# Kernel optimization log

Hardware: AMD Instinct MI355X
Metric: run time of the kernel (lower is better)

The kernel has to match this reference:

```python
import jax, jax.numpy as jnp
import numpy as np

D_MODEL = 1024
D_STATE = 16
EXPAND = 2
D_HEAD = 64
D_CONV = 4
FFN = 2816
NORMALIZE_BC = True
D_INNER = EXPAND * D_MODEL          # 2048
N_HEADS = D_INNER // D_HEAD         # 32
EPS = 1e-6


def _rmsnorm(x, w):
    v = jnp.mean(x * x, axis=-1, keepdims=True)
    return x * jax.lax.rsqrt(v + EPS) * w


def _mixer(x, in_proj_w, conv_w, conv_b, A_log, dt_bias, D, out_proj_w):
    b, l, _ = x.shape
    zxbcdt = x @ in_proj_w.T  # (b, l, 2*D_INNER + 2*D_STATE + N_HEADS)
    z, xBC, dt_raw = jnp.split(zxbcdt, [D_INNER, 2 * D_INNER + 2 * D_STATE], axis=-1)
    # causal depthwise conv over (u, B, C) channels
    xp = jnp.pad(xBC, ((0, 0), (D_CONV - 1, 0), (0, 0)))
    y = conv_b + sum(xp[:, k:k + l, :] * conv_w[:, k] for k in range(D_CONV))
    xBC = jax.nn.silu(y)
    u, Bm, Cm = jnp.split(xBC, [D_INNER, D_INNER + D_STATE], axis=-1)
    if NORMALIZE_BC:
        Bm = Bm / (jnp.linalg.norm(Bm, axis=-1, keepdims=True) + EPS)
        Cm = Cm / (jnp.linalg.norm(Cm, axis=-1, keepdims=True) + EPS)
    dt = jax.nn.softplus(dt_raw + dt_bias)          # (b, l, h)
    A = jnp.exp(A_log)                              # (h, n) oscillator frequencies >= 0
    u = u.reshape(b, l, N_HEADS, D_HEAD)

    # LinOSS implicit (IM) discretization of z' = -A y + B u ; y' = z
    #   S  = 1/(1 + dt^2 A)
    #   w_k = S*(w_{k-1} - dt*A*y_{k-1} + dt*B u_k)
    #   y_k = y_{k-1} + dt*w_k ;  out_k = C y_k + D u_k
    def step(carry, inp):
        w, ys = carry                               # each (b, h, dh, n)
        dt_t, B_t, C_t, u_t = inp                   # (b,h),(b,n),(b,n),(b,h,dh)
        S = 1.0 / (1.0 + (dt_t[:, :, None] ** 2) * A[None])   # (b,h,n)
        Sb = S[:, :, None, :]
        dtb = dt_t[:, :, None, None]
        Ab = A[None, :, None, :]
        Bu = B_t[:, None, None, :] * u_t[..., None]            # (b,h,dh,n)
        w = Sb * (w - dtb * Ab * ys + dtb * Bu)
        ys = ys + dtb * w
        o = jnp.einsum('bhdn,bn->bhd', ys, C_t)
        return (w, ys), o

    init = (jnp.zeros((b, N_HEADS, D_HEAD, D_STATE), x.dtype),
            jnp.zeros((b, N_HEADS, D_HEAD, D_STATE), x.dtype))
    xs = (dt.transpose(1, 0, 2), Bm.transpose(1, 0, 2),
          Cm.transpose(1, 0, 2), u.transpose(1, 0, 2, 3))
    _, ys = jax.lax.scan(step, init, xs)            # (l, b, h, dh)
    ys = ys.transpose(1, 0, 2, 3) + D[None, None, :, None] * u
    out = ys.reshape(b, l, D_INNER) * jax.nn.silu(z)
    return out @ out_proj_w.T


def setup_inputs() -> dict:
    key = jax.random.key(0)
    ks = jax.random.split(key, 12)
    B, L = 4, 2048
    proj_dim = 2 * D_INNER + 2 * D_STATE + N_HEADS
    conv_ch = D_INNER + 2 * D_STATE
    s = lambda k, shape, sc: jax.random.normal(k, shape, jnp.float32) * sc
    return {
        "x": s(ks[0], (B, L, D_MODEL), 1.0),
        "norm1_w": jnp.ones((D_MODEL,), jnp.float32),
        "in_proj_w": s(ks[1], (proj_dim, D_MODEL), D_MODEL ** -0.5),
        "conv_w": s(ks[2], (conv_ch, D_CONV), 0.3),
        "conv_b": jnp.zeros((conv_ch,), jnp.float32),
        "A_log": s(ks[3], (N_HEADS, D_STATE), 0.5),
        "dt_bias": s(ks[4], (N_HEADS,), 0.5),
        "D": s(ks[5], (N_HEADS,), 1.0),
        "out_proj_w": s(ks[6], (D_MODEL, D_INNER), D_INNER ** -0.5),
        "norm2_w": jnp.ones((D_MODEL,), jnp.float32),
        "gate_w": s(ks[7], (FFN, D_MODEL), D_MODEL ** -0.5),
        "up_w": s(ks[8], (FFN, D_MODEL), D_MODEL ** -0.5),
        "down_w": s(ks[9], (D_MODEL, FFN), FFN ** -0.5),
    }


def reference(x, norm1_w, in_proj_w, conv_w, conv_b, A_log, dt_bias, D,
              out_proj_w, norm2_w, gate_w, up_w, down_w):
    h = x + _mixer(_rmsnorm(x, norm1_w), in_proj_w, conv_w, conv_b,
                   A_log, dt_bias, D, out_proj_w)
    hn = _rmsnorm(h, norm2_w)
    ffn = (jax.nn.silu(hn @ gate_w.T) * (hn @ up_w.T)) @ down_w.T
    return h + ffn
```

## Files before the change

### kernel.cpp

```cpp
#include <hip/hip_runtime.h>
#include <hip/hip_bf16.h>

#define D_MODEL   1024
#define D_STATE   16
#define D_HEAD    64
#define D_CONV    4
#define FFN_DIM   2816
#define D_INNER   2048
#define N_HEADS   32
#define BATCH     4
#define SEQ       2048
#define ROWS      (BATCH*SEQ)
#define PROJ_DIM  4160
#define PROJ_PAD  4352
#define CONV_CH   2080
#define CH        128
#define NCH       (SEQ/CH)

typedef __bf16 bf16x8 __attribute__((ext_vector_type(8)));
typedef float  f32x4  __attribute__((ext_vector_type(4)));

__device__ __forceinline__ float siluf(float x) { return x / (1.0f + __expf(-x)); }

#define SBAR() do { asm volatile("" ::: "memory"); __builtin_amdgcn_s_barrier(); asm volatile("" ::: "memory"); } while (0)
#define LGKM0() asm volatile("s_waitcnt lgkmcnt(0)" ::: "memory")
#define VMCNT4() asm volatile("s_waitcnt vmcnt(4)" ::: "memory")
#define VMCNT2() asm volatile("s_waitcnt vmcnt(2)" ::: "memory")
#define VMCNT0() asm volatile("s_waitcnt vmcnt(0)" ::: "memory")

__global__ void cvt_k(const float* __restrict__ src, __hip_bfloat16* __restrict__ dst, int n) {
  int i = blockIdx.x * blockDim.x + threadIdx.x;
  if (i < n) dst[i] = __float2bfloat16(src[i]);
}

__global__ void cvt_pad_k(const float* __restrict__ src, __hip_bfloat16* __restrict__ dst) {
  int i = blockIdx.x * blockDim.x + threadIdx.x;
  if (i >= PROJ_PAD * D_MODEL) return;
  int row = i >> 10;
  dst[i] = (row < PROJ_DIM) ? __float2bfloat16(src[i]) : __float2bfloat16(0.0f);
}

__global__ __launch_bounds__(256) void rmsnorm_k(const float* __restrict__ x,
                                                 const float* __restrict__ w,
                                                 __hip_bfloat16* __restrict__ out,
                                                 float* __restrict__ outf) {
  int row = blockIdx.x;
  int t = threadIdx.x;
  const float* xr = x + (size_t)row * D_MODEL;
  float4 v = ((const float4*)xr)[t];
  float ss = v.x*v.x + v.y*v.y + v.z*v.z + v.w*v.w;
  #pragma unroll
  for (int o = 32; o > 0; o >>= 1) ss += __shfl_xor(ss, o);
  __shared__ float red[4];
  if ((t & 63) == 0) red[t >> 6] = ss;
  __syncthreads();
  ss = red[0] + red[1] + red[2] + red[3];
  float scale = rsqrtf(ss * (1.0f / D_MODEL) + 1e-6f);
  float4 wv = ((const float4*)w)[t];
  float4 r;
  r.x = v.x * scale * wv.x; r.y = v.y * scale * wv.y;
  r.z = v.z * scale * wv.z; r.w = v.w * scale * wv.w;
  __hip_bfloat16* orow = out + (size_t)row * D_MODEL + t * 4;
  orow[0] = __float2bfloat16(r.x);
  orow[1] = __float2bfloat16(r.y);
  orow[2] = __float2bfloat16(r.z);
  orow[3] = __float2bfloat16(r.w);
  if (outf) ((float4*)(outf + (size_t)row * D_MODEL))[t] = r;
}

__global__ __launch_bounds__(256) void dtproj_k(const float* __restrict__ xn,
                                                const float* __restrict__ wi,
                                                const float* __restrict__ dtb,
                                                float* __restrict__ dtT) {
  const int r0 = blockIdx.x * 4;
  const int t  = threadIdx.x;
  const int hh  = t >> 3;
  const int seg = t & 7;

  __shared__ float xs[4][D_MODEL];
  #pragma unroll
  for (int i = 0; i < 4; ++i)
    ((float4*)&xs[i][0])[t] = ((const float4*)(xn + (size_t)(r0 + i) * D_MODEL))[t];
  __syncthreads();

  const float4* w4 = (const float4*)(wi + (size_t)(2 * D_INNER + 2 * D_STATE + hh) * D_MODEL) + seg * 32;
  const float4* x0 = (const float4*)&xs[0][0] + seg * 32;
  const float4* x1 = (const float4*)&xs[1][0] + seg * 32;
  const float4* x2 = (const float4*)&xs[2][0] + seg * 32;
  const float4* x3 = (const float4*)&xs[3][0] + seg * 32;
  float a0 = 0.f, a1 = 0.f, a2 = 0.f, a3 = 0.f;
  #pragma unroll 8
  for (int k = 0; k < 32; ++k) {
    float4 wv = w4[k];
    float4 v0 = x0[k], v1 = x1[k], v2 = x2[k], v3 = x3[k];
    a0 = fmaf(wv.x, v0.x, fmaf(wv.y, v0.y, fmaf(wv.z, v0.z, fmaf(wv.w, v0.w, a0))));
    a1 = fmaf(wv.x, v1.x, fmaf(wv.y, v1.y, fmaf(wv.z, v1.z, fmaf(wv.w, v1.w, a1))));
    a2 = fmaf(wv.x, v2.x, fmaf(wv.y, v2.y, fmaf(wv.z, v2.z, fmaf(wv.w, v2.w, a2))));
    a3 = fmaf(wv.x, v3.x, fmaf(wv.y, v3.y, fmaf(wv.z, v3.z, fmaf(wv.w, v3.w, a3))));
  }
  #pragma unroll
  for (int m = 1; m < 8; m <<= 1) {
    a0 += __shfl_xor(a0, m);
    a1 += __shfl_xor(a1, m);
    a2 += __shfl_xor(a2, m);
    a3 += __shfl_xor(a3, m);
  }
  if (seg == 0) {
    float bias = dtb[hh];
    float v[4] = {a0, a1, a2, a3};
    #pragma unroll
    for (int i = 0; i < 4; ++i) {
      float xv = v[i] + bias;
      dtT[(size_t)hh * ROWS + r0 + i] = (xv > 20.f) ? xv : log1pf(__expf(xv));
    }
  }
}

template<int EPI>
__global__ __launch_bounds__(512, 2) void gemm8(
    const __hip_bfloat16* __restrict__ A,
    const __hip_bfloat16* __restrict__ Bw,
    float* __restrict__ Cf,
    __hip_bfloat16* __restrict__ Cb,
    const float* __restrict__ add_src,
    int M, int N, int K)
{
  extern __shared__ char lds[];
  const int nwg = (M >> 8) * (N >> 8);
  int bid = blockIdx.x;
  bid = (bid & 7) * (nwg >> 3) + (bid >> 3);
  const int ntn = N >> 8;
  const int bm = (bid / ntn) << 8;
  const int bn = (bid % ntn) << 8;

  const int tid  = threadIdx.x;
  const int wid  = tid >> 6;
  const int lane = tid & 63;
  const int wm = wid >> 2;
  const int wn = wid & 3;
  const int r16 = lane & 15;
  const int kg  = lane >> 4;

  const int rb = ((r16 << 6) + (kg << 4)) ^ ((r16 & 8) << 2);

  const int s_sub = tid >> 6;
  const int s_w   = (tid & 63) << 4;
  const int s_wp  = s_w ^ ((((s_w) >> 9) & 1) << 5);
  const int s_row = ((s_sub >> 1) << 4) + (s_wp >> 6);
  const int s_col = ((s_sub & 1) << 5) + ((s_wp >> 1) & 31);

  auto stage = [&](int buf, int mat, int half, int c, int kt) {
    const __hip_bfloat16* src = (mat == 0)
        ? A  + (size_t)(bm + half * 128 + c * 64 + s_row) * K + kt * 64 + s_col
        : Bw + (size_t)(bn + half * 128 + c * 64 + s_row) * K + kt * 64 + s_col;
    char* dst = lds + buf * 65536 + mat * 32768 + half * 16384 + c * 8192 + tid * 16;
    __builtin_amdgcn_global_load_lds((const __attribute__((address_space(1))) unsigned int*)src,
                                     (__attribute__((address_space(3))) unsigned int*)dst,
                                     16, 0, 0);
  };

  f32x4 acc[8][4] = {};
  bf16x8 af[4][2], bfr[4][2];

  const int NT = K >> 6;
  stage(0,0,0,0,0); stage(0,0,0,1,0); stage(0,0,1,0,0); stage(0,0,1,1,0);
  stage(0,1,0,0,0); stage(0,1,0,1,0); stage(0,1,1,0,0); stage(0,1,1,1,0);
  __syncthreads();

  for (int kt = 0; kt < NT; ++kt) {
    const int buf = kt & 1, nbuf = buf ^ 1;
    const bool st = (kt + 1 < NT);
    const char* Ab = lds + buf * 65536 + wm * 16384;
    const char* Bb = lds + buf * 65536 + 32768 + (wn >> 1) * 16384 + (wn & 1) * 8192;

    #pragma unroll
    for (int mi2 = 0; mi2 < 4; ++mi2)
      #pragma unroll
      for (int kk = 0; kk < 2; ++kk)
        af[mi2][kk] = *(const bf16x8*)(Ab + (mi2 * 2 + kk) * 1024 + rb);
    #pragma unroll
    for (int ni = 0; ni < 2; ++ni)
      #pragma unroll
      for (int kk = 0; kk < 2; ++kk)
        bfr[ni][kk] = *(const bf16x8*)(Bb + (ni * 2 + kk) * 1024 + rb);
    if (st) { stage(nbuf,1,0,0,kt+1); stage(nbuf,1,0,1,kt+1); }
    SBAR(); LGKM0();
    __builtin_amdgcn_s_setprio(1);
    #pragma unroll
    for (int mi2 = 0; mi2 < 4; ++mi2)
      #pragma unroll
      for (int ni = 0; ni < 2; ++ni)
        #pragma unroll
        for (int kk = 0; kk < 2; ++kk)
          acc[mi2][ni] = __builtin_amdgcn_mfma_f32_16x16x32_bf16(af[mi2][kk], bfr[ni][kk], acc[mi2][ni], 0, 0, 0);
    __builtin_amdgcn_s_setprio(0);
    SBAR();

    #pragma unroll
    for (int ni = 2; ni < 4; ++ni)
      #pragma unroll
      for (int kk = 0; kk < 2; ++kk)
        bfr[ni][kk] = *(const bf16x8*)(Bb + (ni * 2 + kk) * 1024 + rb);
    if (st) { stage(nbuf,1,1,0,kt+1); stage(nbuf,1,1,1,kt+1); }
    SBAR(); LGKM0();
    __builtin_amdgcn_s_setprio(1);
    #pragma unroll
    for (int mi2 = 0; mi2 < 4; ++mi2)
      #pragma unroll
      for (int ni = 2; ni < 4; ++ni)
        #pragma unroll
        for (int kk = 0; kk < 2; ++kk)
          acc[mi2][ni] = __builtin_amdgcn_mfma_f32_16x16x32_bf16(af[mi2][kk], bfr[ni][kk], acc[mi2][ni], 0, 0, 0);
    __builtin_amdgcn_s_setprio(0);
    if (st) { VMCNT4(); } else { VMCNT0(); }
    SBAR();

    #pragma unroll
    for (int mi2 = 0; mi2 < 4; ++mi2)
      #pragma unroll
      for (int kk = 0; kk < 2; ++kk)
        af[mi2][kk] = *(const bf16x8*)(Ab + ((4 + mi2) * 2 + kk) * 1024 + rb);
    if (st) { stage(nbuf,0,0,0,kt+1); stage(nbuf,0,1,0,kt+1); }
    SBAR(); LGKM0();
    __builtin_amdgcn_s_setprio(1);
    #pragma unroll
    for (int mi2 = 0; mi2 < 4; ++mi2)
      #pragma unroll
      for (int ni = 0; ni < 2; ++ni)
        #pragma unroll
        for (int kk = 0; kk < 2; ++kk)
          acc[4 + mi2][ni] = __builtin_amdgcn_mfma_f32_16x16x32_bf16(af[mi2][kk], bfr[ni][kk], acc[4 + mi2][ni], 0, 0, 0);
    __builtin_amdgcn_s_setprio(0);
    SBAR();

    if (st) { stage(nbuf,0,0,1,kt+1); stage(nbuf,0,1,1,kt+1); }
    SBAR(); LGKM0();
    __builtin_amdgcn_s_setprio(1);
    #pragma unroll
    for (int mi2 = 0; mi2 < 4; ++mi2)
      #pragma unroll
      for (int ni = 2; ni < 4; ++ni)
        #pragma unroll
        for (int kk = 0; kk < 2; ++kk)
          acc[4 + mi2][ni] = __builtin_amdgcn_mfma_f32_16x16x32_bf16(af[mi2][kk], bfr[ni][kk], acc[4 + mi2][ni], 0, 0, 0);
    __builtin_amdgcn_s_setprio(0);
    VMCNT2();
    SBAR();
  }

  #pragma unroll
  for (int mi = 0; mi < 8; ++mi) {
    #pragma unroll
    for (int ni = 0; ni < 4; ++ni) {
      #pragma unroll
      for (int j = 0; j < 4; ++j) {
        int r = bm + wm * 128 + mi * 16 + kg * 4 + j;
        int c = bn + wn * 64 + ni * 16 + r16;
        size_t idx = (size_t)r * N + c;
        float v = acc[mi][ni][j];
        if constexpr (EPI == 0) {
          Cf[idx] = v;
        } else if constexpr (EPI == 1) {
          Cf[idx] = v + add_src[idx];
        } else if constexpr (EPI == 2) {
          Cb[idx] = __float2bfloat16(siluf(v));
        } else if constexpr (EPI == 3) {
          Cb[idx] = __float2bfloat16(v * __bfloat162float(Cb[idx]));
        }
      }
    }
  }
}

template<int EPI>
__global__ __launch_bounds__(512, 2) void gemm8B(
    const __hip_bfloat16* __restrict__ A,
    const __hip_bfloat16* __restrict__ Bw,
    float* __restrict__ Cf,
    __hip_bfloat16* __restrict__ Cb,
    const float* __restrict__ add_src,
    int M, int N, int K)
{
  extern __shared__ char lds[];
  const int nwg = (M >> 8) * (N >> 7);
  int bid = blockIdx.x;
  bid = (bid & 7) * (nwg >> 3) + (bid >> 3);
  const int ntn = N >> 7;
  const int bm = (bid / ntn) << 8;
  const int bn = (bid % ntn) << 7;

  const int tid  = threadIdx.x;
  const int wid  = tid >> 6;
  const int lane = tid & 63;
  const int wm = wid >> 2;
  const int wn = wid & 3;
  const int r16 = lane & 15;
  const int kg  = lane >> 4;

  const int rb = ((r16 << 6) + (kg << 4)) ^ ((r16 & 8) << 2);

  const int s_sub = tid >> 6;
  const int s_w   = (tid & 63) << 4;
  const int s_wp  = s_w ^ ((((s_w) >> 9) & 1) << 5);
  const int s_row = ((s_sub >> 1) << 4) + (s_wp >> 6);
  const int s_col = ((s_sub & 1) << 5) + ((s_wp >> 1) & 31);

  auto stageA = [&](int buf, int half, int c, int kt) {
    const __hip_bfloat16* src = A + (size_t)(bm + half * 128 + c * 64 + s_row) * K + kt * 64 + s_col;
    char* dst = lds + buf * 65536 + half * 16384 + c * 8192 + tid * 16;
    __builtin_amdgcn_global_load_lds((const __attribute__((address_space(1))) unsigned int*)src,
                                     (__attribute__((address_space(3))) unsigned int*)dst,
                                     16, 0, 0);
  };
  auto stageB = [&](int buf, int c, int kt) {
    const __hip_bfloat16* src = Bw + (size_t)(bn + c * 64 + s_row) * K + kt * 64 + s_col;
    char* dst = lds + buf * 65536 + 32768 + c * 8192 + tid * 16;
    __builtin_amdgcn_global_load_lds((const __attribute__((address_space(1))) unsigned int*)src,
                                     (__attribute__((address_space(3))) unsigned int*)dst,
                                     16, 0, 0);
  };

  f32x4 acc[8][2] = {};
  bf16x8 af[4][2], bfr[2][2];

  const int NT = K >> 6;
  stageB(0,0,0); stageB(0,1,0);
  stageA(0,0,0,0); stageA(0,1,0,0); stageA(0,0,1,0); stageA(0,1,1,0);
  __syncthreads();

  for (int kt = 0; kt < NT; ++kt) {
    const int buf = kt & 1, nbuf = buf ^ 1;
    const bool st = (kt + 1 < NT);
    const char* Ab = lds + buf * 65536 + wm * 16384;
    const char* Bb = lds + buf * 65536 + 32768 + (wn >> 1) * 8192 + (wn & 1) * 4096;

    #pragma unroll
    for (int mi2 = 0; mi2 < 4; ++mi2)
      #pragma unroll
      for (int kk = 0; kk < 2; ++kk)
        af[mi2][kk] = *(const bf16x8*)(Ab + (mi2 * 2 + kk) * 1024 + rb);
    #pragma unroll
    for (int ni = 0; ni < 2; ++ni)
      #pragma unroll
      for (int kk = 0; kk < 2; ++kk)
        bfr[ni][kk] = *(const bf16x8*)(Bb + (ni * 2 + kk) * 1024 + rb);
    if (st) { stageB(nbuf,0,kt+1); stageB(nbuf,1,kt+1); stageA(nbuf,0,0,kt+1); stageA(nbuf,1,0,kt+1); }
    SBAR(); LGKM0();
    __builtin_amdgcn_s_setprio(1);
    #pragma unroll
    for (int mi2 = 0; mi2 < 4; ++mi2)
      #pragma unroll
      for (int ni = 0; ni < 2; ++ni)
        #pragma unroll
        for (int kk = 0; kk < 2; ++kk)
          acc[mi2][ni] = __builtin_amdgcn_mfma_f32_16x16x32_bf16(af[mi2][kk], bfr[ni][kk], acc[mi2][ni], 0, 0, 0);
    __builtin_amdgcn_s_setprio(0);
    if (st) { VMCNT4(); } else { VMCNT0(); }
    SBAR();

    #pragma unroll
    for (int mi2 = 0; mi2 < 4; ++mi2)
      #pragma unroll
      for (int kk = 0; kk < 2; ++kk)
        af[mi2][kk] = *(const bf16x8*)(Ab + ((4 + mi2) * 2 + kk) * 1024 + rb);
    if (st) { stageA(nbuf,0,1,kt+1); stageA(nbuf,1,1,kt+1); }
    SBAR(); LGKM0();
    __builtin_amdgcn_s_setprio(1);
    #pragma unroll
    for (int mi2 = 0; mi2 < 4; ++mi2)
      #pragma unroll
      for (int ni = 0; ni < 2; ++ni)
        #pragma unroll
        for (int kk = 0; kk < 2; ++kk)
          acc[4 + mi2][ni] = __builtin_amdgcn_mfma_f32_16x16x32_bf16(af[mi2][kk], bfr[ni][kk], acc[4 + mi2][ni], 0, 0, 0);
    __builtin_amdgcn_s_setprio(0);
    VMCNT2();
    SBAR();
  }

  #pragma unroll
  for (int mi = 0; mi < 8; ++mi) {
    #pragma unroll
    for (int ni = 0; ni < 2; ++ni) {
      #pragma unroll
      for (int j = 0; j < 4; ++j) {
        int r = bm + wm * 128 + mi * 16 + kg * 4 + j;
        int c = bn + wn * 32 + ni * 16 + r16;
        size_t idx = (size_t)r * N + c;
        float v = acc[mi][ni][j];
        if constexpr (EPI == 0) {
          Cf[idx] = v;
        } else if constexpr (EPI == 1) {
          Cf[idx] = v + add_src[idx];
        } else if constexpr (EPI == 2) {
          Cb[idx] = __float2bfloat16(siluf(v));
        } else if constexpr (EPI == 3) {
          Cb[idx] = __float2bfloat16(v * __bfloat162float(Cb[idx]));
        }
      }
    }
  }
}

__global__ __launch_bounds__(256) void bcdt_k(const float* __restrict__ zx,
                                              const float* __restrict__ cw,
                                              const float* __restrict__ cb,
                                              float* __restrict__ bc) {
  int t = threadIdx.x;
  int r = blockIdx.x * 8 + (t >> 5);
  int ch = t & 31;
  int l = r & (SEQ - 1);
  int c = D_INNER + ch;
  float acc = cb[c];
  #pragma unroll
  for (int k = 0; k < 4; ++k) {
    int lp = l - 3 + k;
    if (lp >= 0)
      acc = fmaf(zx[(size_t)(r - 3 + k) * PROJ_PAD + 2 * D_INNER + ch], cw[c * 4 + k], acc);
  }
  acc = siluf(acc);
  float ss = acc * acc;
  ss += __shfl_xor(ss, 1);
  ss += __shfl_xor(ss, 2);
  ss += __shfl_xor(ss, 4);
  ss += __shfl_xor(ss, 8);
  bc[r * 32 + ch] = acc / (sqrtf(ss) + 1e-6f);
}

__global__ __launch_bounds__(256) void pk_k(const float* __restrict__ dtT,
                                            const float* __restrict__ A_log,
                                            float* __restrict__ Pm) {
  int bh = blockIdx.x;
  int h = bh & 31;
  int t = threadIdx.x;
  int ch = t >> 4, n = t & 15;
  float a = __expf(A_log[h * 16 + n]);
  const float* dtp = dtT + (size_t)h * ROWS + (size_t)(bh >> 5) * SEQ + ch * CH;
  float p00 = 1.f, p01 = 0.f, p10 = 0.f, p11 = 1.f;
  for (int l = 0; l < CH; ++l) {
    float dt = dtp[l];
    float s  = 1.0f / fmaf(dt * dt, a, 1.0f);
    float m00 = s;
    float m01 = -dt * a * s;
    float m10 = dt * s;
    float m11 = fmaf(-dt * a, m10, 1.0f);
    float q00 = fmaf(m00, p00, m01 * p10);
    float q01 = fmaf(m00, p01, m01 * p11);
    float q10 = fmaf(m10, p00, m11 * p10);
    float q11 = fmaf(m10, p01, m11 * p11);
    p00 = q00; p01 = q01; p10 = q10; p11 = q11;
  }
  float4 v = {p00, p01, p10, p11};
  *(float4*)&Pm[(((size_t)bh * NCH + ch) * 16 + n) * 4] = v;
}

__global__ __launch_bounds__(256) void prop_k(const float* __restrict__ Pm,
                                              const float* __restrict__ pend,
                                              float* __restrict__ sinit) {
  int gid = blockIdx.x * 256 + threadIdx.x;
  int n  = gid & 15;
  int d  = (gid >> 4) & 63;
  int bh = gid >> 10;
  float s0 = 0.f, s1 = 0.f;
  for (int c = 0; c < NCH; ++c) {
    size_t i2 = (((size_t)bh * NCH + c) * 64 + d) * 16 + n;
    *(float2*)&sinit[i2 * 2] = make_float2(s0, s1);
    float4 P  = *(const float4*)&Pm[(((size_t)bh * NCH + c) * 16 + n) * 4];
    float2 pe = *(const float2*)&pend[i2 * 2];
    float t0 = fmaf(P.x, s0, fmaf(P.y, s1, pe.x));
    float t1 = fmaf(P.z, s0, fmaf(P.w, s1, pe.y));
    s0 = t0; s1 = t1;
  }
}

#define T_TILE 16
#define TPC (CH / T_TILE)
template<int PHASE>
__global__ __launch_bounds__(128) void scan_k(
    const float* __restrict__ zx, const float* __restrict__ bcb,
    const float* __restrict__ dtT, const float* __restrict__ A_log,
    const float* __restrict__ Dp, const float* __restrict__ cw,
    const float* __restrict__ cb, float* __restrict__ states,
    __hip_bfloat16* __restrict__ po)
{
  const int blk  = blockIdx.x;
  const int half = blk & 1;
  const int ch   = (blk >> 1) & 15;
  const int h    = (blk >> 5) & 31;
  const int b    = blk >> 10;
  const int bh   = b * 32 + h;
  const int tid  = threadIdx.x;
  const int wv   = tid >> 6;
  const int lane = tid & 63;
  const int d16  = lane & 15;
  const int ng   = lane >> 4;
  const int n0   = ng * 4;
  const int dl   = half * 32 + wv * 16 + d16;
  const int dcol = h * 64 + dl;
  const size_t rowbase = (size_t)b * SEQ + (size_t)ch * CH;

  __shared__ float xz [2][T_TILE][64];
  __shared__ float bct[2][T_TILE][32];
  __shared__ float st [2][T_TILE][32];
  __shared__ float dtt[2][T_TILE];
  __shared__ float aexp[16];
  __shared__ float opart[T_TILE][32][4];

  if (tid < 16) aexp[tid] = __expf(A_log[h * 16 + tid]);

  const float Dh = Dp[h];
  const float c0 = cw[dcol * 4 + 0], c1 = cw[dcol * 4 + 1];
  const float c2 = cw[dcol * 4 + 2], c3 = cw[dcol * 4 + 3];
  const float cbv = cb[dcol];

  auto stage = [&](int tile, int buf) {
    const size_t r0 = rowbase + (size_t)tile * T_TILE;
    #pragma unroll
    for (int i = 0; i < 2; ++i) {
      int lr = 8 * i + 4 * wv + (lane >> 4);
      int c4 = (lane & 15) * 4;
      int col = (c4 < 32) ? (h * 64 + half * 32 + c4)
                          : (D_INNER + h * 64 + half * 32 + (c4 - 32));
      const float* g = zx + (r0 + lr) * PROJ_PAD + col;
      float* l = &xz[buf][0][0] + (8 * i + 4 * wv) * 64 + (lane & 15) * 4;
      __builtin_amdgcn_global_load_lds((const __attribute__((address_space(1))) unsigned int*)g,
                                       (__attribute__((address_space(3))) unsigned int*)l,
                                       16, 0, 0);
    }
    {
      int lr = 8 * wv + (lane >> 3);
      const float* g = bcb + (r0 + lr) * 32 + (lane & 7) * 4;
      float* l = &bct[buf][0][0] + 8 * wv * 32 + (lane & 7) * 4;
      __builtin_amdgcn_global_load_lds((const __attribute__((address_space(1))) unsigned int*)g,
                                       (__attribute__((address_space(3))) unsigned int*)l,
                                       16, 0, 0);
    }
  };

  auto sprep = [&](int buf, float dtn) {
    #pragma unroll
    for (int i = 0; i < 2; ++i) {
      int idx = tid + 128 * i;
      int row = idx >> 4, n = idx & 15;
      float dv = __shfl(dtn, row);
      float a  = aexp[n];
      st[buf][row][n]      = 1.0f / fmaf(dv * dv, a, 1.0f);
      st[buf][row][16 + n] = dv * a;
    }
  };

  stage(0, 0);
  float dtn = 0.f;
  if (lane < 16) dtn = dtT[(size_t)h * ROWS + rowbase + lane];
  __syncthreads();
  if (tid < 16) dtt[0][tid] = dtn;
  sprep(0, dtn);
  __syncthreads();

  float w[4], ys[4];
  if constexpr (PHASE == 1) {
    #pragma unroll
    for (int j = 0; j < 4; ++j) { w[j] = 0.f; ys[j] = 0.f; }
  } else {
    #pragma unroll
    for (int j = 0; j < 4; ++j) {
      size_t i2 = (((size_t)bh * NCH + ch) * 64 + dl) * 16 + (n0 + j);
      float2 s = *(const float2*)&states[i2 * 2];
      w[j] = s.x; ys[j] = s.y;
    }
  }
  float xw1 = 0.f, xw2 = 0.f, xw3 = 0.f;
  if (ch > 0) {
    const float* xb = zx + rowbase * PROJ_PAD + D_INNER + dcol;
    xw1 = xb[-3 * PROJ_PAD];
    xw2 = xb[-2 * PROJ_PAD];
    xw3 = xb[-1 * PROJ_PAD];
  }
  int cur = 0;

  for (int t = 0; t < TPC; ++t) {
    if (t + 1 < TPC) {
      stage(t + 1, cur ^ 1);
      if (lane < 16) dtn = dtT[(size_t)h * ROWS + rowbase + (size_t)(t + 1) * T_TILE + lane];
    }
    #pragma unroll 4
    for (int l = 0; l < T_TILE; ++l) {
      float xl  = xz[cur][l][32 + wv * 16 + d16];
      float dtv = dtt[cur][l];
      f32x4 Sv = *(const f32x4*)&st [cur][l][n0];
      f32x4 Av = *(const f32x4*)&st [cur][l][16 + n0];
      f32x4 Bv = *(const f32x4*)&bct[cur][l][n0];
      float cacc = fmaf(c3, xl, fmaf(c2, xw3, fmaf(c1, xw2, fmaf(c0, xw1, cbv))));
      float uv = siluf(cacc);
      xw1 = xw2; xw2 = xw3; xw3 = xl;
      float du = dtv * uv;
      if constexpr (PHASE == 3) {
        f32x4 Cv = *(const f32x4*)&bct[cur][l][16 + n0];
        float o = 0.f;
        #pragma unroll
        for (int j = 0; j < 4; ++j) {
          float tmp = fmaf(-Av[j], ys[j], w[j]);
          tmp = fmaf(du, Bv[j], tmp);
          w[j] = Sv[j] * tmp;
          ys[j] = fmaf(dtv, w[j], ys[j]);
          o = fmaf(ys[j], Cv[j], o);
        }
        float ofin = (ng == 0) ? fmaf(Dh, uv, o) : o;
        opart[l][wv * 16 + d16][ng] = ofin;
      } else {
        #pragma unroll
        for (int j = 0; j < 4; ++j) {
          float tmp = fmaf(-Av[j], ys[j], w[j]);
          tmp = fmaf(du, Bv[j], tmp);
          w[j] = Sv[j] * tmp;
          ys[j] = fmaf(dtv, w[j], ys[j]);
        }
      }
    }
    if constexpr (PHASE == 3) {
      #pragma unroll
      for (int i = 0; i < 4; ++i) {
        int l  = (lane >> 4) + 4 * i;
        int dd = wv * 16 + d16;
        f32x4 op = *(const f32x4*)&opart[l][dd][0];
        float zv = xz[cur][l][dd];
        float yv = (op[0] + op[1]) + (op[2] + op[3]);
        po[(rowbase + (size_t)t * T_TILE + l) * D_INNER + (h * 64 + half * 32 + dd)] =
            __float2bfloat16(yv * siluf(zv));
      }
    }
    __syncthreads();
    if (t + 1 < TPC) {
      if (tid < 16) dtt[cur ^ 1][tid] = dtn;
      sprep(cur ^ 1, dtn);
      __syncthreads();
    }
    cur ^= 1;
  }

  if constexpr (PHASE == 1) {
    #pragma unroll
    for (int j = 0; j < 4; ++j) {
      size_t i2 = (((size_t)bh * NCH + ch) * 64 + dl) * 16 + (n0 + j);
      *(float2*)&states[i2 * 2] = make_float2(w[j], ys[j]);
    }
  }
}

extern "C" void kernel_launch(void* const* d_in, const int* in_sizes, int n_in,
                              void* d_out, int out_size, void* d_ws, size_t ws_size,
                              hipStream_t stream) {
  const float* x     = (const float*)d_in[0];
  const float* n1w   = (const float*)d_in[1];
  const float* wi    = (const float*)d_in[2];
  const float* cw    = (const float*)d_in[3];
  const float* cb    = (const float*)d_in[4];
  const float* A_log = (const float*)d_in[5];
  const float* dtb   = (const float*)d_in[6];
  const float* Dp    = (const float*)d_in[7];
  const float* wo    = (const float*)d_in[8];
  const float* n2w   = (const float*)d_in[9];
  const float* wg    = (const float*)d_in[10];
  const float* wu    = (const float*)d_in[11];
  const float* wd    = (const float*)d_in[12];
  float* out = (float*)d_out;

  char* p = (char*)d_ws;
  auto take = [&](size_t b) { char* q = p; p += (b + 255) & ~(size_t)255; return q; };
  __hip_bfloat16* wbi  = (__hip_bfloat16*)take((size_t)PROJ_PAD * D_MODEL * 2);
  __hip_bfloat16* wbo  = (__hip_bfloat16*)take((size_t)D_MODEL * D_INNER * 2);
  __hip_bfloat16* wbg  = (__hip_bfloat16*)take((size_t)FFN_DIM * D_MODEL * 2);
  __hip_bfloat16* wbu  = (__hip_bfloat16*)take((size_t)FFN_DIM * D_MODEL * 2);
  __hip_bfloat16* wbd  = (__hip_bfloat16*)take((size_t)D_MODEL * FFN_DIM * 2);
  __hip_bfloat16* h0b  = (__hip_bfloat16*)take((size_t)ROWS * D_MODEL * 2);
  float*          zx   = (float*)take((size_t)ROWS * PROJ_PAD * 4);
  float*          bcb  = (float*)take((size_t)ROWS * 32 * 4);
  float*          dtT  = (float*)take((size_t)ROWS * 32 * 4);
  __hip_bfloat16* po   = (__hip_bfloat16*)take((size_t)ROWS * D_INNER * 2);
  float*          pend = (float*)take((size_t)128 * NCH * 64 * 16 * 2 * 4);
  float*          sini = (float*)take((size_t)128 * NCH * 64 * 16 * 2 * 4);
  float*          Pm   = (float*)take((size_t)128 * NCH * 16 * 4 * 4);
  float*          h0f  = (float*)zx;
  float*          h    = (float*)zx;
  __hip_bfloat16* gact = (__hip_bfloat16*)((char*)zx + 33554432);

  hipFuncSetAttribute(reinterpret_cast<const void*>(&gemm8<0>),  hipFuncAttributeMaxDynamicSharedMemorySize, 131072);
  hipFuncSetAttribute(reinterpret_cast<const void*>(&gemm8<2>),  hipFuncAttributeMaxDynamicSharedMemorySize, 131072);
  hipFuncSetAttribute(reinterpret_cast<const void*>(&gemm8<3>),  hipFuncAttributeMaxDynamicSharedMemorySize, 131072);
  hipFuncSetAttribute(reinterpret_cast<const void*>(&gemm8B<1>), hipFuncAttributeMaxDynamicSharedMemorySize, 131072);

  cvt_pad_k<<<(PROJ_PAD * D_MODEL + 255) / 256, 256, 0, stream>>>(wi, wbi);
  cvt_k<<<(D_MODEL * D_INNER + 255) / 256, 256, 0, stream>>>(wo, wbo, D_MODEL * D_INNER);
  cvt_k<<<(FFN_DIM * D_MODEL + 255) / 256, 256, 0, stream>>>(wg, wbg, FFN_DIM * D_MODEL);
  cvt_k<<<(FFN_DIM * D_MODEL + 255) / 256, 256, 0, stream>>>(wu, wbu, FFN_DIM * D_MODEL);
  cvt_k<<<(FFN_DIM * D_MODEL + 255) / 256, 256, 0, stream>>>(wd, wbd, FFN_DIM * D_MODEL);

  rmsnorm_k<<<ROWS, 256, 0, stream>>>(x, n1w, h0b, h0f);
  dtproj_k<<<ROWS / 4, 256, 0, stream>>>(h0f, wi, dtb, dtT);
  gemm8<0><<<(ROWS / 256) * (PROJ_PAD / 256), 512, 131072, stream>>>(h0b, wbi, zx, nullptr, nullptr,
                                                                     ROWS, PROJ_PAD, D_MODEL);
  bcdt_k<<<ROWS / 8, 256, 0, stream>>>(zx, cw, cb, bcb);
  pk_k<<<BATCH * N_HEADS, 256, 0, stream>>>(dtT, A_log, Pm);
  scan_k<1><<<BATCH * N_HEADS * NCH * 2, 128, 0, stream>>>(zx, bcb, dtT, A_log, Dp, cw, cb, pend, nullptr);
  prop_k<<<BATCH * N_HEADS * 64 * 16 / 256, 256, 0, stream>>>(Pm, pend, sini);
  scan_k<3><<<BATCH * N_HEADS * NCH * 2, 128, 0, stream>>>(zx, bcb, dtT, A_log, Dp, cw, cb, sini, po);
  gemm8B<1><<<(ROWS / 256) * (D_MODEL / 128), 512, 131072, stream>>>(po, wbo, h, nullptr, x,
                                                                     ROWS, D_MODEL, D_INNER);
  rmsnorm_k<<<ROWS, 256, 0, stream>>>(h, n2w, h0b, nullptr);
  gemm8<2><<<(ROWS / 256) * (FFN_DIM / 256), 512, 131072, stream>>>(h0b, wbg, nullptr, gact, nullptr,
                                                                    ROWS, FFN_DIM, D_MODEL);
  gemm8<3><<<(ROWS / 256) * (FFN_DIM / 256), 512, 131072, stream>>>(h0b, wbu, nullptr, gact, nullptr,
                                                                    ROWS, FFN_DIM, D_MODEL);
  gemm8B<1><<<(ROWS / 256) * (D_MODEL / 128), 512, 131072, stream>>>(gact, wbd, out, nullptr, h,
                                                                     ROWS, D_MODEL, FFN_DIM);
}
```

Baseline: 711.5 us.

## Precompute conv+SiLU of u into bf16 buffer and simplify scan staging

Adds a standalone kernel that computes the causal depthwise conv and SiLU for the u channels once and stores the result as bf16 in the output buffer. Both scan phases then stage that bf16 u instead of recomputing the conv from fp32 projection columns, and phase 1 no longer loads z at all. The scan also keeps exp(A) in registers instead of in shared memory and uses packed two-wide float math for the recurrence. In exchange it adds an extra pass over the projection output, rounds u to bf16 before the recurrence, and reuses the output buffer in place for both u and the result.

```diff
diff --git a/kernel.cpp b/kernel.cpp
--- a/kernel.cpp
+++ b/kernel.cpp
@@ -19,6 +19,7 @@
 
 typedef __bf16 bf16x8 __attribute__((ext_vector_type(8)));
 typedef float  f32x4  __attribute__((ext_vector_type(4)));
+typedef float  f32x2  __attribute__((ext_vector_type(2)));
 
 __device__ __forceinline__ float siluf(float x) { return x / (1.0f + __expf(-x)); }
 
@@ -400,6 +401,39 @@
       }
     }
   }
+}
+
+__global__ __launch_bounds__(256) void duconv_k(const float* __restrict__ zx,
+                                                const float* __restrict__ cw,
+                                                const float* __restrict__ cb,
+                                                __hip_bfloat16* __restrict__ u_po) {
+  int idx = blockIdx.x * 256 + threadIdx.x;
+  int q = idx & 511;
+  int r = idx >> 9;
+  int d0 = q << 2;
+  int l = r & (SEQ - 1);
+  float4 cb4 = ((const float4*)cb)[q];
+  float tw[4][4];
+  #pragma unroll
+  for (int i = 0; i < 4; ++i) {
+    float4 t = ((const float4*)cw)[d0 + i];
+    tw[i][0] = t.x; tw[i][1] = t.y; tw[i][2] = t.z; tw[i][3] = t.w;
+  }
+  float a[4] = {cb4.x, cb4.y, cb4.z, cb4.w};
+  #pragma unroll
+  for (int k = 0; k < 4; ++k) {
+    if (l - 3 + k >= 0) {
+      float4 xv = *(const float4*)(zx + (size_t)(r - 3 + k) * PROJ_PAD + D_INNER + d0);
+      a[0] = fmaf(xv.x, tw[0][k], a[0]);
+      a[1] = fmaf(xv.y, tw[1][k], a[1]);
+      a[2] = fmaf(xv.z, tw[2][k], a[2]);
+      a[3] = fmaf(xv.w, tw[3][k], a[3]);
+    }
+  }
+  union { ushort4 u4; __hip_bfloat16 b[4]; } pk;
+  #pragma unroll
+  for (int i = 0; i < 4; ++i) pk.b[i] = __float2bfloat16(siluf(a[i]));
+  *(ushort4*)(u_po + (size_t)r * D_INNER + d0) = pk.u4;
 }
 
 __global__ __launch_bounds__(256) void bcdt_k(const float* __restrict__ zx,
@@ -479,9 +513,8 @@
 __global__ __launch_bounds__(128) void scan_k(
     const float* __restrict__ zx, const float* __restrict__ bcb,
     const float* __restrict__ dtT, const float* __restrict__ A_log,
-    const float* __restrict__ Dp, const float* __restrict__ cw,
-    const float* __restrict__ cb, float* __restrict__ states,
-    __hip_bfloat16* __restrict__ po)
+    const float* __restrict__ Dp, float* __restrict__ states,
+    __hip_bfloat16* u_po)
 {
   const int blk  = blockIdx.x;
   const int half = blk & 1;
@@ -495,45 +528,67 @@
   const int d16  = lane & 15;
   const int ng   = lane >> 4;
   const int n0   = ng * 4;
-  const int dl   = half * 32 + wv * 16 + d16;
-  const int dcol = h * 64 + dl;
+  const int dwv  = wv * 16 + d16;
+  const int dl   = half * 32 + dwv;
+  const int dbase = h * 64 + half * 32;
   const size_t rowbase = (size_t)b * SEQ + (size_t)ch * CH;
 
-  __shared__ float xz [2][T_TILE][64];
-  __shared__ float bct[2][T_TILE][32];
-  __shared__ float st [2][T_TILE][32];
+  __shared__ __hip_bfloat16 dut[2][T_TILE][32];
+  __shared__ float Btl[2][T_TILE][16];
+  __shared__ float Ctl[PHASE == 3 ? 2 : 1][T_TILE][16];
+  __shared__ float zt [PHASE == 3 ? 2 : 1][T_TILE][32];
+  __shared__ float st [2][T_TILE][16];
   __shared__ float dtt[2][T_TILE];
   __shared__ float aexp[16];
-  __shared__ float opart[T_TILE][32][4];
+  __shared__ float opart[PHASE == 3 ? T_TILE : 1][32][4];
 
   if (tid < 16) aexp[tid] = __expf(A_log[h * 16 + tid]);
 
+  f32x2 A2[2];
+  #pragma unroll
+  for (int k = 0; k < 2; ++k) {
+    A2[k][0] = __expf(A_log[h * 16 + n0 + 2 * k]);
+    A2[k][1] = __expf(A_log[h * 16 + n0 + 2 * k + 1]);
+  }
   const float Dh = Dp[h];
-  const float c0 = cw[dcol * 4 + 0], c1 = cw[dcol * 4 + 1];
-  const float c2 = cw[dcol * 4 + 2], c3 = cw[dcol * 4 + 3];
-  const float cbv = cb[dcol];
 
   auto stage = [&](int tile, int buf) {
     const size_t r0 = rowbase + (size_t)tile * T_TILE;
-    #pragma unroll
-    for (int i = 0; i < 2; ++i) {
-      int lr = 8 * i + 4 * wv + (lane >> 4);
-      int c4 = (lane & 15) * 4;
-      int col = (c4 < 32) ? (h * 64 + half * 32 + c4)
-                          : (D_INNER + h * 64 + half * 32 + (c4 - 32));
-      const float* g = zx + (r0 + lr) * PROJ_PAD + col;
-      float* l = &xz[buf][0][0] + (8 * i + 4 * wv) * 64 + (lane & 15) * 4;
-      __builtin_amdgcn_global_load_lds((const __attribute__((address_space(1))) unsigned int*)g,
-                                       (__attribute__((address_space(3))) unsigned int*)l,
-                                       16, 0, 0);
-    }
-    {
-      int lr = 8 * wv + (lane >> 3);
-      const float* g = bcb + (r0 + lr) * 32 + (lane & 7) * 4;
-      float* l = &bct[buf][0][0] + 8 * wv * 32 + (lane & 7) * 4;
-      __builtin_amdgcn_global_load_lds((const __attribute__((address_space(1))) unsigned int*)g,
-                                       (__attribute__((address_space(3))) unsigned int*)l,
-                                       16, 0, 0);
+    if constexpr (PHASE == 3) {
+      {
+        int row = wv * 8 + (lane >> 3);
+        const float* g = zx + (r0 + row) * PROJ_PAD + dbase + (lane & 7) * 4;
+        float* l_ = &zt[buf][0][0] + wv * 256 + lane * 4;
+        __builtin_amdgcn_global_load_lds((const __attribute__((address_space(1))) unsigned int*)g,
+                                         (__attribute__((address_space(3))) unsigned int*)l_, 16, 0, 0);
+      }
+      if (wv == 0) {
+        const __hip_bfloat16* g = u_po + (r0 + (lane >> 2)) * D_INNER + dbase + (lane & 3) * 8;
+        __hip_bfloat16* l_ = &dut[buf][0][0] + lane * 8;
+        __builtin_amdgcn_global_load_lds((const __attribute__((address_space(1))) unsigned int*)g,
+                                         (__attribute__((address_space(3))) unsigned int*)l_, 16, 0, 0);
+      } else {
+        const float* gB = bcb + (r0 + (lane >> 2)) * 32 + (lane & 3) * 4;
+        float* lB = &Btl[buf][0][0] + lane * 4;
+        __builtin_amdgcn_global_load_lds((const __attribute__((address_space(1))) unsigned int*)gB,
+                                         (__attribute__((address_space(3))) unsigned int*)lB, 16, 0, 0);
+        const float* gC = bcb + (r0 + (lane >> 2)) * 32 + 16 + (lane & 3) * 4;
+        float* lC = &Ctl[buf][0][0] + lane * 4;
+        __builtin_amdgcn_global_load_lds((const __attribute__((address_space(1))) unsigned int*)gC,
+                                         (__attribute__((address_space(3))) unsigned int*)lC, 16, 0, 0);
+      }
+    } else {
+      if (wv == 0) {
+        const __hip_bfloat16* g = u_po + (r0 + (lane >> 2)) * D_INNER + dbase + (lane & 3) * 8;
+        __hip_bfloat16* l_ = &dut[buf][0][0] + lane * 8;
+        __builtin_amdgcn_global_load_lds((const __attribute__((address_space(1))) unsigned int*)g,
+                                         (__attribute__((address_space(3))) unsigned int*)l_, 16, 0, 0);
+      } else {
+        const float* gB = bcb + (r0 + (lane >> 2)) * 32 + (lane & 3) * 4;
+        float* lB = &Btl[buf][0][0] + lane * 4;
+        __builtin_amdgcn_global_load_lds((const __attribute__((address_space(1))) unsigned int*)gB,
+                                         (__attribute__((address_space(3))) unsigned int*)lB, 16, 0, 0);
+      }
     }
   };
 
@@ -544,8 +599,7 @@
       int row = idx >> 4, n = idx & 15;
       float dv = __shfl(dtn, row);
       float a  = aexp[n];
-      st[buf][row][n]      = 1.0f / fmaf(dv * dv, a, 1.0f);
-      st[buf][row][16 + n] = dv * a;
+      st[buf][row][n] = 1.0f / fmaf(dv * dv, a, 1.0f);
     }
   };
 
@@ -557,24 +611,19 @@
   sprep(0, dtn);
   __syncthreads();
 
-  float w[4], ys[4];
+  f32x2 w2[2], ys2[2];
   if constexpr (PHASE == 1) {
     #pragma unroll
-    for (int j = 0; j < 4; ++j) { w[j] = 0.f; ys[j] = 0.f; }
+    for (int k = 0; k < 2; ++k) { w2[k] = (f32x2){0.f, 0.f}; ys2[k] = (f32x2){0.f, 0.f}; }
   } else {
     #pragma unroll
-    for (int j = 0; j < 4; ++j) {
-      size_t i2 = (((size_t)bh * NCH + ch) * 64 + dl) * 16 + (n0 + j);
-      float2 s = *(const float2*)&states[i2 * 2];
-      w[j] = s.x; ys[j] = s.y;
-    }
-  }
-  float xw1 = 0.f, xw2 = 0.f, xw3 = 0.f;
-  if (ch > 0) {
-    const float* xb = zx + rowbase * PROJ_PAD + D_INNER + dcol;
-    xw1 = xb[-3 * PROJ_PAD];
-    xw2 = xb[-2 * PROJ_PAD];
-    xw3 = xb[-1 * PROJ_PAD];
+    for (int k = 0; k < 2; ++k)
+      #pragma unroll
+      for (int j = 0; j < 2; ++j) {
+        size_t i2 = (((size_t)bh * NCH + ch) * 64 + dl) * 16 + (n0 + 2 * k + j);
+        float2 s = *(const float2*)&states[i2 * 2];
+        w2[k][j] = s.x; ys2[k][j] = s.y;
+      }
   }
   int cur = 0;
 
@@ -585,35 +634,37 @@
     }
     #pragma unroll 4
     for (int l = 0; l < T_TILE; ++l) {
-      float xl  = xz[cur][l][32 + wv * 16 + d16];
+      float uv  = __bfloat162float(dut[cur][l][dwv]);
       float dtv = dtt[cur][l];
-      f32x4 Sv = *(const f32x4*)&st [cur][l][n0];
-      f32x4 Av = *(const f32x4*)&st [cur][l][16 + n0];
-      f32x4 Bv = *(const f32x4*)&bct[cur][l][n0];
-      float cacc = fmaf(c3, xl, fmaf(c2, xw3, fmaf(c1, xw2, fmaf(c0, xw1, cbv))));
-      float uv = siluf(cacc);
-      xw1 = xw2; xw2 = xw3; xw3 = xl;
+      f32x4 Sv4 = *(const f32x4*)&st [cur][l][n0];
+      f32x4 Bv4 = *(const f32x4*)&Btl[cur][l][n0];
       float du = dtv * uv;
+      f32x2 S2[2] = { {Sv4[0], Sv4[1]}, {Sv4[2], Sv4[3]} };
+      f32x2 B2[2] = { {Bv4[0], Bv4[1]}, {Bv4[2], Bv4[3]} };
       if constexpr (PHASE == 3) {
-        f32x4 Cv = *(const f32x4*)&bct[cur][l][16 + n0];
-        float o = 0.f;
+        f32x4 Cv4 = *(const f32x4*)&Ctl[cur][l][n0];
+        f32x2 C2[2] = { {Cv4[0], Cv4[1]}, {Cv4[2], Cv4[3]} };
+        f32x2 o2 = {0.f, 0.f};
         #pragma unroll
-        for (int j = 0; j < 4; ++j) {
-          float tmp = fmaf(-Av[j], ys[j], w[j]);
-          tmp = fmaf(du, Bv[j], tmp);
-          w[j] = Sv[j] * tmp;
-          ys[j] = fmaf(dtv, w[j], ys[j]);
-          o = fmaf(ys[j], Cv[j], o);
+        for (int k = 0; k < 2; ++k) {
+          f32x2 dtA = dtv * A2[k];
+          f32x2 tmp = w2[k] - dtA * ys2[k];
+          tmp = tmp + du * B2[k];
+          w2[k] = S2[k] * tmp;
+          ys2[k] = ys2[k] + dtv * w2[k];
+          o2 = o2 + ys2[k] * C2[k];
         }
+        float o = o2[0] + o2[1];
         float ofin = (ng == 0) ? fmaf(Dh, uv, o) : o;
-        opart[l][wv * 16 + d16][ng] = ofin;
+        opart[l][dwv][ng] = ofin;
       } else {
         #pragma unroll
-        for (int j = 0; j < 4; ++j) {
-          float tmp = fmaf(-Av[j], ys[j], w[j]);
-          tmp = fmaf(du, Bv[j], tmp);
-          w[j] = Sv[j] * tmp;
-          ys[j] = fmaf(dtv, w[j], ys[j]);
+        for (int k = 0; k < 2; ++k) {
+          f32x2 dtA = dtv * A2[k];
+          f32x2 tmp = w2[k] - dtA * ys2[k];
+          tmp = tmp + du * B2[k];
+          w2[k] = S2[k] * tmp;
+          ys2[k] = ys2[k] + dtv * w2[k];
         }
       }
     }
@@ -623,9 +674,9 @@
         int l  = (lane >> 4) + 4 * i;
         int dd = wv * 16 + d16;
         f32x4 op = *(const f32x4*)&opart[l][dd][0];
-        float zv = xz[cur][l][dd];
+        float zv = zt[cur][l][dd];
         float yv = (op[0] + op[1]) + (op[2] + op[3]);
-        po[(rowbase + (size_t)t * T_TILE + l) * D_INNER + (h * 64 + half * 32 + dd)] =
+        u_po[(rowbase + (size_t)t * T_TILE + l) * D_INNER + dbase + dd] =
             __float2bfloat16(yv * siluf(zv));
       }
     }
@@ -640,10 +691,12 @@
 
   if constexpr (PHASE == 1) {
     #pragma unroll
-    for (int j = 0; j < 4; ++j) {
-      size_t i2 = (((size_t)bh * NCH + ch) * 64 + dl) * 16 + (n0 + j);
-      *(float2*)&states[i2 * 2] = make_float2(w[j], ys[j]);
-    }
+    for (int k = 0; k < 2; ++k)
+      #pragma unroll
+      for (int j = 0; j < 2; ++j) {
+        size_t i2 = (((size_t)bh * NCH + ch) * 64 + dl) * 16 + (n0 + 2 * k + j);
+        *(float2*)&states[i2 * 2] = make_float2(w2[k][j], ys2[k][j]);
+      }
   }
 }
 
@@ -699,11 +752,12 @@
   dtproj_k<<<ROWS / 4, 256, 0, stream>>>(h0f, wi, dtb, dtT);
   gemm8<0><<<(ROWS / 256) * (PROJ_PAD / 256), 512, 131072, stream>>>(h0b, wbi, zx, nullptr, nullptr,
                                                                      ROWS, PROJ_PAD, D_MODEL);
+  duconv_k<<<ROWS * 512 / 256, 256, 0, stream>>>(zx, cw, cb, po);
   bcdt_k<<<ROWS / 8, 256, 0, stream>>>(zx, cw, cb, bcb);
   pk_k<<<BATCH * N_HEADS, 256, 0, stream>>>(dtT, A_log, Pm);
-  scan_k<1><<<BATCH * N_HEADS * NCH * 2, 128, 0, stream>>>(zx, bcb, dtT, A_log, Dp, cw, cb, pend, nullptr);
+  scan_k<1><<<BATCH * N_HEADS * NCH * 2, 128, 0, stream>>>(zx, bcb, dtT, A_log, Dp, pend, po);
   prop_k<<<BATCH * N_HEADS * 64 * 16 / 256, 256, 0, stream>>>(Pm, pend, sini);
-  scan_k<3><<<BATCH * N_HEADS * NCH * 2, 128, 0, stream>>>(zx, bcb, dtT, A_log, Dp, cw, cb, sini, po);
+  scan_k<3><<<BATCH * N_HEADS * NCH * 2, 128, 0, stream>>>(zx, bcb, dtT, A_log, Dp, sini, po);
   gemm8B<1><<<(ROWS / 256) * (D_MODEL / 128), 512, 131072, stream>>>(po, wbo, h, nullptr, x,
                                                                      ROWS, D_MODEL, D_INNER);
   rmsnorm_k<<<ROWS, 256, 0, stream>>>(h, n2w, h0b, nullptr);
```

Result: no change. 704.1 us (-1.0%).
